# Kernel tuning notes

Hardware: AMD Instinct MI355X
Metric: run time of the kernel (lower is better)

Reference implementation:

```python
import jax, jax.numpy as jnp
import numpy as np

B, L, H, N, CIN, COUT, U = 32, 12, 12, 2048, 2, 1, 64
K3 = 3  # num_matrices = n_supports * max_diffusion_step + 1 = 1*2 + 1


def setup_inputs() -> dict:
    rng = np.random.default_rng(0)
    # random sparse-ish symmetric adjacency -> scaled laplacian support (lambda_max ~= 2)
    A = rng.random((N, N), dtype=np.float32)
    A = np.maximum(A, A.T)
    A = A * (A > 0.995)
    d = A.sum(axis=1)
    dis = 1.0 / np.sqrt(np.maximum(d, 1e-6))
    Lap = np.eye(N, dtype=np.float32) - (dis[:, None] * A) * dis[None, :]
    support = (Lap - np.eye(N, dtype=np.float32)).astype(np.float32)  # 2/lmax*L - I with lmax=2

    key = jax.random.key(0)
    ks = jax.random.split(key, 6)

    def w(k, shape, fan):
        return jax.random.normal(k, shape, jnp.float32) / np.float32(np.sqrt(fan))

    Cg_e = (CIN + U) * K3   # 198
    Cg_d = (COUT + U) * K3  # 195
    return {
        "history_data": jax.random.normal(ks[0], (B, L, N, CIN), jnp.float32),
        "support": jnp.asarray(support),
        "enc_Wg": w(ks[1], (Cg_e, 2 * U), Cg_e),
        "enc_bg": jnp.ones((2 * U,), jnp.float32),  # gate bias starts at 1.0 (original repo)
        "enc_Wc": w(ks[2], (Cg_e, U), Cg_e),
        "enc_bc": jnp.zeros((U,), jnp.float32),
        "dec_Wg": w(ks[3], (Cg_d, 2 * U), Cg_d),
        "dec_bg": jnp.ones((2 * U,), jnp.float32),
        "dec_Wc": w(ks[4], (Cg_d, U), Cg_d),
        "dec_bc": jnp.zeros((U,), jnp.float32),
        "Wp": w(ks[5], (U, COUT), U),
        "bp": jnp.zeros((COUT,), jnp.float32),
    }


def _gconv(support, x, W, b):
    # x: [B, N, C]; Chebyshev diffusion T0=x, T1=Sx, T2=2S(Sx)-x, stacked feature-major
    x1 = jnp.einsum('mn,bnc->bmc', support, x)
    x2 = 2.0 * jnp.einsum('mn,bnc->bmc', support, x1) - x
    xs = jnp.stack([x, x1, x2], axis=-1)  # [B, N, C, 3]
    b_, n_, c_, k_ = xs.shape
    y = xs.reshape(b_ * n_, c_ * k_) @ W + b
    return y.reshape(b_, n_, -1)


def _cell(support, x, h, Wg, bg, Wc, bc):
    # DCGRU cell: x [B,N,in], h [B,N,U]
    cat = jnp.concatenate([x, h], axis=-1)
    ru = jax.nn.sigmoid(_gconv(support, cat, Wg, bg))
    r, u = jnp.split(ru, 2, axis=-1)
    c = jnp.tanh(_gconv(support, jnp.concatenate([x, r * h], axis=-1), Wc, bc))
    return u * h + (1.0 - u) * c


def reference(history_data, support, enc_Wg, enc_bg, enc_Wc, enc_bc,
              dec_Wg, dec_bg, dec_Wc, dec_bc, Wp, bp):
    hist = jnp.transpose(history_data, (1, 0, 2, 3))  # [L, B, N, CIN]
    h0 = jnp.zeros((B, N, U), history_data.dtype)

    def enc_step(h, xt):
        return _cell(support, xt, h, enc_Wg, enc_bg, enc_Wc, enc_bc), None

    h_enc, _ = jax.lax.scan(enc_step, h0, hist)

    go = jnp.zeros((B, N, COUT), history_data.dtype)

    def dec_step(carry, _):
        h, xin = carry
        h = _cell(support, xin, h, dec_Wg, dec_bg, dec_Wc, dec_bc)
        out = (h.reshape(-1, U) @ Wp + bp).reshape(B, N, COUT)
        return (h, out), out

    _, outs = jax.lax.scan(dec_step, (h_enc, go), None, length=H)  # [H, B, N, COUT]
    return jnp.transpose(outs, (1, 0, 2, 3))  # [B, H, N, COUT]
```

## Files before the change

kernel.cpp:

```cpp
#include <hip/hip_runtime.h>
#include <math.h>

#define NN 2048
#define BB 32
#define LL 12
#define HHH 12
#define UU 64
#define STR 68
#define SLAB (BB*STR)
#define SEGP (SLAB/4)
#define MR (NN*BB)
#define CSR_CAP 262144
#define PACK_HALF 28672

typedef short bfrag __attribute__((ext_vector_type(8)));
typedef float ffrag __attribute__((ext_vector_type(4)));

__device__ __forceinline__ unsigned packsf(float x) {
  unsigned u = __float_as_uint(x);
  unsigned hb = (u + 0x7FFFu + ((u >> 16) & 1u)) & 0xFFFF0000u;
  float rem = x - __uint_as_float(hb);
  unsigned lb = __float_as_uint(rem) >> 16;
  return hb | lb;
}
__device__ __forceinline__ float recsf(unsigned u) {
  return __uint_as_float(u & 0xFFFF0000u) + __uint_as_float(u << 16);
}
__device__ __forceinline__ float sigm(float x) { return 1.0f / (1.0f + __expf(-x)); }
__device__ __forceinline__ float tanhfast(float x) {
  float e = __expf(2.0f * x);
  return 1.0f - 2.0f / (e + 1.0f);
}

__global__ __launch_bounds__(256) void k_row_count(const float* __restrict__ S, int* __restrict__ cnt) {
  int m = blockIdx.x;
  const float* row = S + (size_t)m * NN;
  int c = 0;
  for (int i = threadIdx.x; i < NN; i += 256) c += (row[i] != 0.0f);
  __shared__ int sm[4];
  for (int off = 32; off; off >>= 1) c += __shfl_down(c, off, 64);
  if ((threadIdx.x & 63) == 0) sm[threadIdx.x >> 6] = c;
  __syncthreads();
  if (threadIdx.x == 0) cnt[m] = sm[0] + sm[1] + sm[2] + sm[3];
}

__global__ __launch_bounds__(256) void k_scan(const int* __restrict__ cnt, int* __restrict__ rp) {
  __shared__ int tot[256];
  int t = threadIdx.x;
  int base = t * 8;
  int v[8]; int s = 0;
  #pragma unroll
  for (int k = 0; k < 8; ++k) { v[k] = cnt[base + k]; s += v[k]; }
  tot[t] = s;
  __syncthreads();
  for (int off = 1; off < 256; off <<= 1) {
    int add = (t >= off) ? tot[t - off] : 0;
    __syncthreads();
    tot[t] += add;
    __syncthreads();
  }
  int run = (t == 0) ? 0 : tot[t - 1];
  #pragma unroll
  for (int k = 0; k < 8; ++k) { rp[base + k] = run; run += v[k]; }
  if (t == 255) rp[NN] = run;
}

__global__ __launch_bounds__(256) void k_fill(const float* __restrict__ S, const int* __restrict__ rp,
                                              int* __restrict__ cols, float* __restrict__ vals) {
  int m = blockIdx.x;
  const float* row = S + (size_t)m * NN;
  __shared__ int wsum[4];
  __shared__ int chunkbase;
  if (threadIdx.x == 0) chunkbase = rp[m];
  __syncthreads();
  int lane = threadIdx.x & 63, w = threadIdx.x >> 6;
  for (int ch = 0; ch < NN / 256; ++ch) {
    int i = ch * 256 + threadIdx.x;
    float val = row[i];
    bool p = (val != 0.0f);
    unsigned long long mask = __ballot(p);
    int rank = __popcll(mask & ((1ull << lane) - 1ull));
    if (lane == 0) wsum[w] = __popcll(mask);
    __syncthreads();
    int off = 0;
    for (int q = 0; q < w; ++q) off += wsum[q];
    if (p) { int k = chunkbase + off + rank; cols[k] = i; vals[k] = val; }
    __syncthreads();
    if (threadIdx.x == 0) chunkbase += wsum[0] + wsum[1] + wsum[2] + wsum[3];
    __syncthreads();
  }
}

__global__ __launch_bounds__(256) void k_pack(const float* __restrict__ Wsrc, unsigned short* __restrict__ dst,
                                              int CIN_, int NO) {
  int idx = blockIdx.x * 256 + threadIdx.x;
  int nh_count = NO >> 6;
  int tot = nh_count * 7 * 4 * 64 * 8;
  if (idx >= tot) return;
  int j = idx & 7;
  int r1 = idx >> 3;  int lane = r1 & 63;
  int r2 = r1 >> 6;   int nf = r2 & 3;
  int r3 = r2 >> 2;   int ks = r3 % 7; int nh = r3 / 7;
  int grp = lane >> 4, l15 = lane & 15;
  int col = nh*64 + nf*16 + l15;
  float wv = 0.0f;
  if (ks < 6) {
    int kb = ks >> 1;
    int c = CIN_ + (ks & 1)*32 + grp*8 + j;
    wv = Wsrc[((size_t)c*3 + kb)*NO + col];
  } else {
    int q = grp*8 + j;
    if (q < 3*CIN_) { int kb = q / CIN_, c = q % CIN_; wv = Wsrc[((size_t)c*3 + kb)*NO + col]; }
  }
  unsigned pw = packsf(wv);
  size_t basehi = ((size_t)nh*PACK_HALF) + ((((size_t)ks*4 + nf)*2 + 0)*64 + lane)*8 + j;
  size_t baselo = ((size_t)nh*PACK_HALF) + ((((size_t)ks*4 + nf)*2 + 1)*64 + lane)*8 + j;
  dst[basehi] = (unsigned short)(pw >> 16);
  dst[baselo] = (unsigned short)(pw & 0xFFFFu);
}

__global__ __launch_bounds__(256) void k_packt(const float* __restrict__ src, unsigned* __restrict__ dst, int n) {
  int i = blockIdx.x * 256 + threadIdx.x;
  if (i < n) dst[i] = packsf(src[i]);
}

template<int SRC, int X0M>
__global__ __launch_bounds__(256, 4) void k_hop(
    const int* __restrict__ rp, const int* __restrict__ cols, const float* __restrict__ vals,
    const unsigned* __restrict__ src, const unsigned* __restrict__ xP,
    const unsigned* __restrict__ hP, const unsigned* __restrict__ x0p,
    unsigned* __restrict__ Y, int t) {
  __shared__ int   scol[64];
  __shared__ float sval[64];
  int orig = blockIdx.x;
  int swz = (orig & 7) * 1024 + (orig >> 3);
  int seg = swz >> 11;
  int node = swz & 2047;
  int j0 = rp[node], j1 = rp[node + 1];
  int tid = threadIdx.x;
  int w0 = seg * SEGP + tid, w1 = w0 + 256, w2 = w0 + 512;
  bool a2 = tid < (SEGP - 512);
  float acc0 = 0.f, acc1 = 0.f, acc2 = 0.f;

  int b0 = 0, c0 = 0, b1 = 0, c1 = 0, b2 = 0, c2 = 0;
  if constexpr (SRC != 0 || X0M > 0) {
    b0 = w0 / STR; c0 = w0 - b0 * STR;
    b1 = w1 / STR; c1 = w1 - b1 * STR;
    b2 = w2 / STR; c2 = w2 - b2 * STR;
  }

  const unsigned *bp0, *bp1, *bp2;
  unsigned st0, st1, st2;
  bool z0 = false, z1 = false, z2 = false;
  if constexpr (SRC == 0) {
    bp0 = src + w0; bp1 = src + w1; bp2 = src + (a2 ? w2 : w0);
    st0 = SLAB; st1 = SLAB; st2 = SLAB;
    z2 = !a2;
  } else {
    auto mk = [&](int b, int c, const unsigned*& bp, unsigned& st, bool& zz) {
      if (c < 64) { bp = hP + (size_t)b * UU + c; st = BB * UU; }
      else if (SRC == 1 && c < 66) { bp = xP + ((size_t)(b * LL + t)) * NN * 2 + (c - 64); st = 2; }
      else if (SRC == 2 && c == 64) { bp = xP + b; st = BB; }
      else { bp = hP; st = 0; zz = true; }
    };
    mk(b0, c0, bp0, st0, z0);
    mk(b1, c1, bp1, st1, z1);
    if (a2) mk(b2, c2, bp2, st2, z2);
    else { bp2 = hP; st2 = 0; z2 = true; }
  }

  for (int base = j0; base < j1; base += 64) {
    int cnt = min(64, j1 - base);
    if (tid < cnt) { scol[tid] = cols[base + tid]; sval[tid] = vals[base + tid]; }
    __syncthreads();
    int jj = 0;
    for (; jj + 4 <= cnt; jj += 4) {
      unsigned uv[12];
      float sv[4];
      #pragma unroll
      for (int q = 0; q < 4; ++q) {
        unsigned n = (unsigned)scol[jj + q];
        sv[q] = sval[jj + q];
        uv[q*3+0] = bp0[(size_t)(n * st0)];
        uv[q*3+1] = bp1[(size_t)(n * st1)];
        uv[q*3+2] = bp2[(size_t)(n * st2)];
      }
      #pragma unroll
      for (int q = 0; q < 4; ++q) {
        acc0 = fmaf(sv[q], recsf(z0 ? 0u : uv[q*3+0]), acc0);
        acc1 = fmaf(sv[q], recsf(z1 ? 0u : uv[q*3+1]), acc1);
        acc2 = fmaf(sv[q], recsf(z2 ? 0u : uv[q*3+2]), acc2);
      }
    }
    for (; jj < cnt; ++jj) {
      unsigned n = (unsigned)scol[jj]; float s = sval[jj];
      unsigned a = bp0[(size_t)(n * st0)];
      unsigned b = bp1[(size_t)(n * st1)];
      unsigned c = bp2[(size_t)(n * st2)];
      acc0 = fmaf(s, recsf(z0 ? 0u : a), acc0);
      acc1 = fmaf(s, recsf(z1 ? 0u : b), acc1);
      acc2 = fmaf(s, recsf(z2 ? 0u : c), acc2);
    }
    __syncthreads();
  }

  unsigned* yr = Y + (size_t)node * SLAB;
  if constexpr (X0M < 0) {
    yr[w0] = packsf(acc0);
    yr[w1] = packsf(acc1);
    if (a2) yr[w2] = packsf(acc2);
  } else {
    auto X0V = [&](int wq, int b, int c) -> float {
      if constexpr (X0M == 0) {
        return recsf(x0p[(size_t)node * SLAB + wq]);
      } else if constexpr (X0M == 1) {
        if (c < 64) return recsf(hP[((size_t)node * BB + b) * UU + c]);
        if (c < 66) return recsf(xP[(((size_t)(b * LL + t)) * NN + node) * 2 + (c - 64)]);
        return 0.f;
      } else {
        if (c < 64) return recsf(hP[((size_t)node * BB + b) * UU + c]);
        if (c == 64) return recsf(xP[(size_t)node * BB + b]);
        return 0.f;
      }
    };
    yr[w0] = packsf(2.f * acc0 - X0V(w0, b0, c0));
    yr[w1] = packsf(2.f * acc1 - X0V(w1, b1, c1));
    if (a2) yr[w2] = packsf(2.f * acc2 - X0V(w2, b2, c2));
  }
}

template<int CATM>
__global__ __launch_bounds__(256, 4) void k_gate(
    const unsigned* __restrict__ hP, const unsigned* __restrict__ xP,
    const unsigned* __restrict__ T1P, const unsigned* __restrict__ T2P,
    const unsigned short* __restrict__ Bpack, const float* __restrict__ bg,
    unsigned* __restrict__ zP, float* __restrict__ Ug, int t) {
  int tid = threadIdx.x;
  int r0 = blockIdx.x * 64;
  int w = tid >> 6, lane = tid & 63, grp = lane >> 4, l15 = lane & 15;
  int row0 = r0 + w*16 + l15;
  ffrag acc[8];
  #pragma unroll
  for (int nf = 0; nf < 8; ++nf) acc[nf] = (ffrag){0.f, 0.f, 0.f, 0.f};

  #pragma unroll
  for (int ks = 0; ks < 7; ++ks) {
    int ko = (ks & 1)*32 + grp*8;
    bfrag ah0, al0;
    if (ks < 6) {
      const unsigned* p0; int st;
      if (ks < 2)      { p0 = hP;  st = UU; }
      else if (ks < 4) { p0 = T1P; st = STR; }
      else             { p0 = T2P; st = STR; }
      const unsigned* a0 = p0 + (size_t)row0*st + ko;
      uint4 q00 = *(const uint4*)a0, q01 = *(const uint4*)(a0 + 4);
      unsigned ua0[8] = {q00.x,q00.y,q00.z,q00.w,q01.x,q01.y,q01.z,q01.w};
      #pragma unroll
      for (int jj = 0; jj < 8; ++jj) {
        ah0[jj] = (short)(ua0[jj] >> 16); al0[jj] = (short)(ua0[jj] & 0xFFFFu);
      }
    } else {
      unsigned ua0[8] = {0,0,0,0,0,0,0,0};
      if (grp == 0) {
        if (CATM == 1) {
          int n0r = row0 >> 5, b0r = row0 & 31;
          const unsigned* hx0 = xP + (((size_t)(b0r*LL + t))*NN + n0r)*2;
          ua0[0] = hx0[0]; ua0[1] = hx0[1];
          ua0[2] = T1P[(size_t)row0*STR + 64]; ua0[3] = T1P[(size_t)row0*STR + 65];
          ua0[4] = T2P[(size_t)row0*STR + 64]; ua0[5] = T2P[(size_t)row0*STR + 65];
        } else {
          ua0[0] = xP[row0];
          ua0[1] = T1P[(size_t)row0*STR + 64];
          ua0[2] = T2P[(size_t)row0*STR + 64];
        }
      }
      #pragma unroll
      for (int jj = 0; jj < 8; ++jj) {
        ah0[jj] = (short)(ua0[jj] >> 16); al0[jj] = (short)(ua0[jj] & 0xFFFFu);
      }
    }
    #pragma unroll
    for (int nf = 0; nf < 8; ++nf) {
      const unsigned short* bb = Bpack + (size_t)(nf >> 2)*PACK_HALF
                               + (((size_t)(ks*4 + (nf & 3))*2)*64 + lane)*8;
      bfrag bh = *(const bfrag*)bb;
      bfrag bl = *(const bfrag*)(bb + 512);
      acc[nf] = __builtin_amdgcn_mfma_f32_16x16x32_bf16(ah0, bh, acc[nf], 0, 0, 0);
      acc[nf] = __builtin_amdgcn_mfma_f32_16x16x32_bf16(ah0, bl, acc[nf], 0, 0, 0);
      acc[nf] = __builtin_amdgcn_mfma_f32_16x16x32_bf16(al0, bh, acc[nf], 0, 0, 0);
    }
  }
  float bgv[8];
  #pragma unroll
  for (int nf = 0; nf < 8; ++nf) bgv[nf] = bg[nf*16 + l15];
  #pragma unroll
  for (int reg = 0; reg < 4; ++reg) {
    int row = r0 + w*16 + grp*4 + reg;
    #pragma unroll
    for (int nf = 0; nf < 8; ++nf) {
      int col = nf*16 + l15;
      float v = sigm(acc[nf][reg] + bgv[nf]);
      if (col < 64) {
        float ho = recsf(hP[(size_t)row*UU + col]);
        zP[(size_t)row*STR + col] = packsf(v * ho);
      } else {
        Ug[(size_t)row*UU + (col - 64)] = v;
      }
    }
  }
  if (l15 == 0) {
    #pragma unroll
    for (int reg = 0; reg < 4; ++reg) {
      int row = r0 + w*16 + grp*4 + reg;
      size_t zb = (size_t)row*STR;
      if (CATM == 1) {
        int n = row >> 5, b = row & 31;
        const unsigned* hx = xP + (((size_t)(b*LL + t))*NN + n)*2;
        zP[zb + 64] = hx[0]; zP[zb + 65] = hx[1];
      } else {
        zP[zb + 64] = xP[row]; zP[zb + 65] = 0u;
      }
      zP[zb + 66] = 0u; zP[zb + 67] = 0u;
    }
  }
}

template<bool DEC>
__global__ __launch_bounds__(256, 4) void k_cand(
    const unsigned* __restrict__ zP, const unsigned* __restrict__ T1P,
    const unsigned* __restrict__ T2P,
    const unsigned short* __restrict__ Bpack, const float* __restrict__ bc,
    const float* __restrict__ Ug, const unsigned* __restrict__ hOld,
    unsigned* __restrict__ hNew,
    const float* __restrict__ Wp, const float* __restrict__ bp,
    float* __restrict__ out, unsigned* __restrict__ xioP, int t) {
  int tid = threadIdx.x;
  int r0 = blockIdx.x * 64;
  int w = tid >> 6, lane = tid & 63, grp = lane >> 4, l15 = lane & 15;
  int row0 = r0 + w*16 + l15;
  ffrag acc[4];
  #pragma unroll
  for (int nf = 0; nf < 4; ++nf) acc[nf] = (ffrag){0.f, 0.f, 0.f, 0.f};

  #pragma unroll
  for (int ks = 0; ks < 7; ++ks) {
    int ko = (ks & 1)*32 + grp*8;
    bfrag ah0, al0;
    if (ks < 6) {
      const unsigned* p0;
      if (ks < 2)      p0 = zP;
      else if (ks < 4) p0 = T1P;
      else             p0 = T2P;
      const unsigned* a0 = p0 + (size_t)row0*STR + ko;
      uint4 q00 = *(const uint4*)a0, q01 = *(const uint4*)(a0 + 4);
      unsigned ua0[8] = {q00.x,q00.y,q00.z,q00.w,q01.x,q01.y,q01.z,q01.w};
      #pragma unroll
      for (int jj = 0; jj < 8; ++jj) {
        ah0[jj] = (short)(ua0[jj] >> 16); al0[jj] = (short)(ua0[jj] & 0xFFFFu);
      }
    } else {
      unsigned ua0[8] = {0,0,0,0,0,0,0,0};
      if (grp == 0) {
        if (!DEC) {
          ua0[0] = zP[(size_t)row0*STR + 64];  ua0[1] = zP[(size_t)row0*STR + 65];
          ua0[2] = T1P[(size_t)row0*STR + 64]; ua0[3] = T1P[(size_t)row0*STR + 65];
          ua0[4] = T2P[(size_t)row0*STR + 64]; ua0[5] = T2P[(size_t)row0*STR + 65];
        } else {
          ua0[0] = zP[(size_t)row0*STR + 64];
          ua0[1] = T1P[(size_t)row0*STR + 64];
          ua0[2] = T2P[(size_t)row0*STR + 64];
        }
      }
      #pragma unroll
      for (int jj = 0; jj < 8; ++jj) {
        ah0[jj] = (short)(ua0[jj] >> 16); al0[jj] = (short)(ua0[jj] & 0xFFFFu);
      }
    }
    #pragma unroll
    for (int nf = 0; nf < 4; ++nf) {
      const unsigned short* bb = Bpack + (((size_t)(ks*4 + nf)*2)*64 + lane)*8;
      bfrag bh = *(const bfrag*)bb;
      bfrag bl = *(const bfrag*)(bb + 512);
      acc[nf] = __builtin_amdgcn_mfma_f32_16x16x32_bf16(ah0, bh, acc[nf], 0, 0, 0);
      acc[nf] = __builtin_amdgcn_mfma_f32_16x16x32_bf16(ah0, bl, acc[nf], 0, 0, 0);
      acc[nf] = __builtin_amdgcn_mfma_f32_16x16x32_bf16(al0, bh, acc[nf], 0, 0, 0);
    }
  }
  float bcv[4], wpv[4];
  #pragma unroll
  for (int nf = 0; nf < 4; ++nf) {
    bcv[nf] = bc[nf*16 + l15];
    wpv[nf] = DEC ? Wp[nf*16 + l15] : 0.f;
  }
  float bp0 = DEC ? bp[0] : 0.f;
  #pragma unroll
  for (int reg = 0; reg < 4; ++reg) {
    int row = r0 + w*16 + grp*4 + reg;
    float p = 0.f;
    #pragma unroll
    for (int nf = 0; nf < 4; ++nf) {
      int col = nf*16 + l15;
      float cf = tanhfast(acc[nf][reg] + bcv[nf]);
      float u  = Ug[(size_t)row*UU + col];
      float ho = recsf(hOld[(size_t)row*UU + col]);
      float hv = u * ho + (1.0f - u) * cf;
      hNew[(size_t)row*UU + col] = packsf(hv);
      if (DEC) p = fmaf(hv, wpv[nf], p);
    }
    if (DEC) {
      p += __shfl_xor(p, 1, 64);
      p += __shfl_xor(p, 2, 64);
      p += __shfl_xor(p, 4, 64);
      p += __shfl_xor(p, 8, 64);
      if (l15 == 0) {
        float val = p + bp0;
        int n = row >> 5, b = row & 31;
        out[((size_t)b*HHH + t)*NN + n] = val;
        xioP[row] = packsf(val);
      }
    }
  }
}

extern "C" void kernel_launch(void* const* d_in, const int* in_sizes, int n_in,
                              void* d_out, int out_size, void* d_ws, size_t ws_size,
                              hipStream_t stream) {
  (void)in_sizes; (void)n_in; (void)out_size; (void)ws_size;
  const float* hist = (const float*)d_in[0];
  const float* support = (const float*)d_in[1];
  const float* eWg = (const float*)d_in[2];
  const float* ebg = (const float*)d_in[3];
  const float* eWc = (const float*)d_in[4];
  const float* ebc = (const float*)d_in[5];
  const float* dWg = (const float*)d_in[6];
  const float* dbg = (const float*)d_in[7];
  const float* dWc = (const float*)d_in[8];
  const float* dbc = (const float*)d_in[9];
  const float* Wp  = (const float*)d_in[10];
  const float* bp  = (const float*)d_in[11];
  float* out = (float*)d_out;

  char* base = (char*)d_ws;
  size_t off = 0;
  auto carve = [&](size_t bytes) -> void* {
    void* p = base + off;
    off += (bytes + 255) & ~(size_t)255;
    return p;
  };
  int*   cnt   = (int*)carve(NN * 4);
  int*   rpB   = (int*)carve((NN + 1) * 4);
  int*   colsB = (int*)carve(CSR_CAP * 4);
  float* valsB = (float*)carve(CSR_CAP * 4);
  unsigned short* Pge = (unsigned short*)carve(2 * PACK_HALF * 2);
  unsigned short* Pgd = (unsigned short*)carve(2 * PACK_HALF * 2);
  unsigned short* Pce = (unsigned short*)carve((size_t)PACK_HALF * 2);
  unsigned short* Pcd = (unsigned short*)carve((size_t)PACK_HALF * 2);
  unsigned* histP = (unsigned*)carve((size_t)BB * LL * NN * 2 * 4);
  unsigned* T1P   = (unsigned*)carve((size_t)NN * SLAB * 4);
  unsigned* T2P   = (unsigned*)carve((size_t)NN * SLAB * 4);
  unsigned* zP    = (unsigned*)carve((size_t)NN * SLAB * 4);
  float*    UgF   = (float*)carve((size_t)MR * UU * 4);
  unsigned* hPa   = (unsigned*)carve((size_t)MR * UU * 4);
  unsigned* hPb   = (unsigned*)carve((size_t)MR * UU * 4);
  unsigned* xioP  = (unsigned*)carve((size_t)MR * 4);

  hipMemsetAsync(hPa, 0, (size_t)MR * UU * 4, stream);
  hipMemsetAsync(xioP, 0, (size_t)MR * 4, stream);

  k_row_count<<<NN, 256, 0, stream>>>(support, cnt);
  k_scan<<<1, 256, 0, stream>>>(cnt, rpB);
  k_fill<<<NN, 256, 0, stream>>>(support, rpB, colsB, valsB);
  k_pack<<<112, 256, 0, stream>>>(eWg, Pge, 2, 128);
  k_pack<<<56, 256, 0, stream>>>(eWc, Pce, 2, 64);
  k_pack<<<112, 256, 0, stream>>>(dWg, Pgd, 1, 128);
  k_pack<<<56, 256, 0, stream>>>(dWc, Pcd, 1, 64);
  k_packt<<<(BB*LL*NN*2 + 255)/256, 256, 0, stream>>>(hist, histP, BB*LL*NN*2);

  unsigned* hc = hPa; unsigned* hn = hPb;
  for (int t = 0; t < LL; ++t) {
    k_hop<1,-1><<<8192, 256, 0, stream>>>(rpB, colsB, valsB, nullptr, histP, hc, nullptr, T1P, t);
    k_hop<0, 1><<<8192, 256, 0, stream>>>(rpB, colsB, valsB, T1P, histP, hc, nullptr, T2P, t);
    k_gate<1><<<MR/64, 256, 0, stream>>>(hc, histP, T1P, T2P, Pge, ebg, zP, UgF, t);
    k_hop<0,-1><<<8192, 256, 0, stream>>>(rpB, colsB, valsB, zP, nullptr, nullptr, nullptr, T1P, t);
    k_hop<0, 0><<<8192, 256, 0, stream>>>(rpB, colsB, valsB, T1P, nullptr, nullptr, zP, T2P, t);
    k_cand<false><<<MR/64, 256, 0, stream>>>(zP, T1P, T2P, Pce, ebc, UgF, hc, hn,
                                             Wp, bp, out, xioP, t);
    unsigned* tmp = hc; hc = hn; hn = tmp;
  }
  for (int t = 0; t < HHH; ++t) {
    k_hop<2,-1><<<8192, 256, 0, stream>>>(rpB, colsB, valsB, nullptr, xioP, hc, nullptr, T1P, t);
    k_hop<0, 2><<<8192, 256, 0, stream>>>(rpB, colsB, valsB, T1P, xioP, hc, nullptr, T2P, t);
    k_gate<2><<<MR/64, 256, 0, stream>>>(hc, xioP, T1P, T2P, Pgd, dbg, zP, UgF, t);
    k_hop<0,-1><<<8192, 256, 0, stream>>>(rpB, colsB, valsB, zP, nullptr, nullptr, nullptr, T1P, t);
    k_hop<0, 0><<<8192, 256, 0, stream>>>(rpB, colsB, valsB, T1P, nullptr, nullptr, zP, T2P, t);
    k_cand<true><<<MR/64, 256, 0, stream>>>(zP, T1P, T2P, Pcd, dbc, UgF, hc, hn,
                                            Wp, bp, out, xioP, t);
    unsigned* tmp = hc; hc = hn; hn = tmp;
  }
}
```

Baseline: 3.971 ms.

## Fold Chebyshev 2Sx-x into packed weights and split hop into eight segments

The second diffusion hop now writes plain S·(Sx) rather than 2S(Sx)-x. The identity term and the factor of two are folded into the packed weight matrix: the T0 weight becomes W0-W2 and the T2 weight becomes 2·W2. This removes the per-element x0 reload and subtraction from the hop kernels. Separately, each node's slab is split into 8 segments instead of 4, giving 16384 blocks with two columns per thread and an 8-deep gather unroll. The goal is more parallelism and more memory-level parallelism, at the cost of more blocks re-reading the CSR row.

```diff
diff --git a/kernel.cpp b/kernel.cpp
--- a/kernel.cpp
+++ b/kernel.cpp
@@ -8,7 +8,8 @@
 #define UU 64
 #define STR 68
 #define SLAB (BB*STR)
-#define SEGP (SLAB/4)
+#define SEGS 8
+#define SEGW (SLAB/SEGS)
 #define MR (NN*BB)
 #define CSR_CAP 262144
 #define PACK_HALF 28672
@@ -104,13 +105,19 @@
   int grp = lane >> 4, l15 = lane & 15;
   int col = nh*64 + nf*16 + l15;
   float wv = 0.0f;
+  int kb = -1, c = 0;
   if (ks < 6) {
-    int kb = ks >> 1;
-    int c = CIN_ + (ks & 1)*32 + grp*8 + j;
-    wv = Wsrc[((size_t)c*3 + kb)*NO + col];
+    kb = ks >> 1;
+    c = CIN_ + (ks & 1)*32 + grp*8 + j;
   } else {
     int q = grp*8 + j;
-    if (q < 3*CIN_) { int kb = q / CIN_, c = q % CIN_; wv = Wsrc[((size_t)c*3 + kb)*NO + col]; }
+    if (q < 3*CIN_) { kb = q / CIN_; c = q % CIN_; }
+  }
+  if (kb >= 0) {
+    float w0 = Wsrc[((size_t)c*3 + 0)*NO + col];
+    float w1 = Wsrc[((size_t)c*3 + 1)*NO + col];
+    float w2 = Wsrc[((size_t)c*3 + 2)*NO + col];
+    wv = (kb == 0) ? (w0 - w2) : ((kb == 1) ? w1 : 2.0f*w2);
   }
   unsigned pw = packsf(wv);
   size_t basehi = ((size_t)nh*PACK_HALF) + ((((size_t)ks*4 + nf)*2 + 0)*64 + lane)*8 + j;
@@ -124,49 +131,41 @@
   if (i < n) dst[i] = packsf(src[i]);
 }
 
-template<int SRC, int X0M>
+template<int SRC>
 __global__ __launch_bounds__(256, 4) void k_hop(
     const int* __restrict__ rp, const int* __restrict__ cols, const float* __restrict__ vals,
     const unsigned* __restrict__ src, const unsigned* __restrict__ xP,
-    const unsigned* __restrict__ hP, const unsigned* __restrict__ x0p,
-    unsigned* __restrict__ Y, int t) {
+    const unsigned* __restrict__ hP, unsigned* __restrict__ Y, int t) {
   __shared__ int   scol[64];
   __shared__ float sval[64];
   int orig = blockIdx.x;
-  int swz = (orig & 7) * 1024 + (orig >> 3);
+  int swz = (orig & 7) * 2048 + (orig >> 3);
   int seg = swz >> 11;
   int node = swz & 2047;
   int j0 = rp[node], j1 = rp[node + 1];
   int tid = threadIdx.x;
-  int w0 = seg * SEGP + tid, w1 = w0 + 256, w2 = w0 + 512;
-  bool a2 = tid < (SEGP - 512);
-  float acc0 = 0.f, acc1 = 0.f, acc2 = 0.f;
-
-  int b0 = 0, c0 = 0, b1 = 0, c1 = 0, b2 = 0, c2 = 0;
-  if constexpr (SRC != 0 || X0M > 0) {
-    b0 = w0 / STR; c0 = w0 - b0 * STR;
-    b1 = w1 / STR; c1 = w1 - b1 * STR;
-    b2 = w2 / STR; c2 = w2 - b2 * STR;
-  }
-
-  const unsigned *bp0, *bp1, *bp2;
-  unsigned st0, st1, st2;
-  bool z0 = false, z1 = false, z2 = false;
+  int w0 = seg * SEGW + tid;
+  bool a1 = tid < (SEGW - 256);
+  int w1 = w0 + 256;
+  float acc0 = 0.f, acc1 = 0.f;
+
+  const unsigned *bp0, *bp1;
+  unsigned st0, st1;
+  bool z0 = false, z1 = false;
   if constexpr (SRC == 0) {
-    bp0 = src + w0; bp1 = src + w1; bp2 = src + (a2 ? w2 : w0);
-    st0 = SLAB; st1 = SLAB; st2 = SLAB;
-    z2 = !a2;
+    bp0 = src + w0; st0 = SLAB;
+    bp1 = src + (a1 ? w1 : w0); st1 = SLAB; z1 = !a1;
   } else {
-    auto mk = [&](int b, int c, const unsigned*& bp, unsigned& st, bool& zz) {
+    auto mk = [&](int wq, const unsigned*& bp, unsigned& st, bool& zz) {
+      int b = wq / STR, c = wq - b * STR;
       if (c < 64) { bp = hP + (size_t)b * UU + c; st = BB * UU; }
       else if (SRC == 1 && c < 66) { bp = xP + ((size_t)(b * LL + t)) * NN * 2 + (c - 64); st = 2; }
       else if (SRC == 2 && c == 64) { bp = xP + b; st = BB; }
       else { bp = hP; st = 0; zz = true; }
     };
-    mk(b0, c0, bp0, st0, z0);
-    mk(b1, c1, bp1, st1, z1);
-    if (a2) mk(b2, c2, bp2, st2, z2);
-    else { bp2 = hP; st2 = 0; z2 = true; }
+    mk(w0, bp0, st0, z0);
+    if (a1) mk(w1, bp1, st1, z1);
+    else { bp1 = hP; st1 = 0; z1 = true; }
   }
 
   for (int base = j0; base < j1; base += 64) {
@@ -174,59 +173,34 @@
     if (tid < cnt) { scol[tid] = cols[base + tid]; sval[tid] = vals[base + tid]; }
     __syncthreads();
     int jj = 0;
-    for (; jj + 4 <= cnt; jj += 4) {
-      unsigned uv[12];
-      float sv[4];
-      #pragma unroll
-      for (int q = 0; q < 4; ++q) {
+    for (; jj + 8 <= cnt; jj += 8) {
+      unsigned u0[8], u1[8];
+      float sv[8];
+      #pragma unroll
+      for (int q = 0; q < 8; ++q) {
         unsigned n = (unsigned)scol[jj + q];
         sv[q] = sval[jj + q];
-        uv[q*3+0] = bp0[(size_t)(n * st0)];
-        uv[q*3+1] = bp1[(size_t)(n * st1)];
-        uv[q*3+2] = bp2[(size_t)(n * st2)];
-      }
-      #pragma unroll
-      for (int q = 0; q < 4; ++q) {
-        acc0 = fmaf(sv[q], recsf(z0 ? 0u : uv[q*3+0]), acc0);
-        acc1 = fmaf(sv[q], recsf(z1 ? 0u : uv[q*3+1]), acc1);
-        acc2 = fmaf(sv[q], recsf(z2 ? 0u : uv[q*3+2]), acc2);
+        u0[q] = bp0[(size_t)(n * st0)];
+        u1[q] = bp1[(size_t)(n * st1)];
+      }
+      #pragma unroll
+      for (int q = 0; q < 8; ++q) {
+        acc0 = fmaf(sv[q], recsf(z0 ? 0u : u0[q]), acc0);
+        acc1 = fmaf(sv[q], recsf(z1 ? 0u : u1[q]), acc1);
       }
     }
     for (; jj < cnt; ++jj) {
       unsigned n = (unsigned)scol[jj]; float s = sval[jj];
       unsigned a = bp0[(size_t)(n * st0)];
       unsigned b = bp1[(size_t)(n * st1)];
-      unsigned c = bp2[(size_t)(n * st2)];
       acc0 = fmaf(s, recsf(z0 ? 0u : a), acc0);
       acc1 = fmaf(s, recsf(z1 ? 0u : b), acc1);
-      acc2 = fmaf(s, recsf(z2 ? 0u : c), acc2);
-    }
-    __syncthreads();
-  }
-
+    }
+    __syncthreads();
+  }
   unsigned* yr = Y + (size_t)node * SLAB;
-  if constexpr (X0M < 0) {
-    yr[w0] = packsf(acc0);
-    yr[w1] = packsf(acc1);
-    if (a2) yr[w2] = packsf(acc2);
-  } else {
-    auto X0V = [&](int wq, int b, int c) -> float {
-      if constexpr (X0M == 0) {
-        return recsf(x0p[(size_t)node * SLAB + wq]);
-      } else if constexpr (X0M == 1) {
-        if (c < 64) return recsf(hP[((size_t)node * BB + b) * UU + c]);
-        if (c < 66) return recsf(xP[(((size_t)(b * LL + t)) * NN + node) * 2 + (c - 64)]);
-        return 0.f;
-      } else {
-        if (c < 64) return recsf(hP[((size_t)node * BB + b) * UU + c]);
-        if (c == 64) return recsf(xP[(size_t)node * BB + b]);
-        return 0.f;
-      }
-    };
-    yr[w0] = packsf(2.f * acc0 - X0V(w0, b0, c0));
-    yr[w1] = packsf(2.f * acc1 - X0V(w1, b1, c1));
-    if (a2) yr[w2] = packsf(2.f * acc2 - X0V(w2, b2, c2));
-  }
+  yr[w0] = packsf(acc0);
+  if (a1) yr[w1] = packsf(acc1);
 }
 
 template<int CATM>
@@ -478,21 +452,21 @@
 
   unsigned* hc = hPa; unsigned* hn = hPb;
   for (int t = 0; t < LL; ++t) {
-    k_hop<1,-1><<<8192, 256, 0, stream>>>(rpB, colsB, valsB, nullptr, histP, hc, nullptr, T1P, t);
-    k_hop<0, 1><<<8192, 256, 0, stream>>>(rpB, colsB, valsB, T1P, histP, hc, nullptr, T2P, t);
+    k_hop<1><<<NN*SEGS, 256, 0, stream>>>(rpB, colsB, valsB, nullptr, histP, hc, T1P, t);
+    k_hop<0><<<NN*SEGS, 256, 0, stream>>>(rpB, colsB, valsB, T1P, nullptr, nullptr, T2P, t);
     k_gate<1><<<MR/64, 256, 0, stream>>>(hc, histP, T1P, T2P, Pge, ebg, zP, UgF, t);
-    k_hop<0,-1><<<8192, 256, 0, stream>>>(rpB, colsB, valsB, zP, nullptr, nullptr, nullptr, T1P, t);
-    k_hop<0, 0><<<8192, 256, 0, stream>>>(rpB, colsB, valsB, T1P, nullptr, nullptr, zP, T2P, t);
+    k_hop<0><<<NN*SEGS, 256, 0, stream>>>(rpB, colsB, valsB, zP, nullptr, nullptr, T1P, t);
+    k_hop<0><<<NN*SEGS, 256, 0, stream>>>(rpB, colsB, valsB, T1P, nullptr, nullptr, T2P, t);
     k_cand<false><<<MR/64, 256, 0, stream>>>(zP, T1P, T2P, Pce, ebc, UgF, hc, hn,
                                              Wp, bp, out, xioP, t);
     unsigned* tmp = hc; hc = hn; hn = tmp;
   }
   for (int t = 0; t < HHH; ++t) {
-    k_hop<2,-1><<<8192, 256, 0, stream>>>(rpB, colsB, valsB, nullptr, xioP, hc, nullptr, T1P, t);
-    k_hop<0, 2><<<8192, 256, 0, stream>>>(rpB, colsB, valsB, T1P, xioP, hc, nullptr, T2P, t);
+    k_hop<2><<<NN*SEGS, 256, 0, stream>>>(rpB, colsB, valsB, nullptr, xioP, hc, T1P, t);
+    k_hop<0><<<NN*SEGS, 256, 0, stream>>>(rpB, colsB, valsB, T1P, nullptr, nullptr, T2P, t);
     k_gate<2><<<MR/64, 256, 0, stream>>>(hc, xioP, T1P, T2P, Pgd, dbg, zP, UgF, t);
-    k_hop<0,-1><<<8192, 256, 0, stream>>>(rpB, colsB, valsB, zP, nullptr, nullptr, nullptr, T1P, t);
-    k_hop<0, 0><<<8192, 256, 0, stream>>>(rpB, colsB, valsB, T1P, nullptr, nullptr, zP, T2P, t);
+    k_hop<0><<<NN*SEGS, 256, 0, stream>>>(rpB, colsB, valsB, zP, nullptr, nullptr, T1P, t);
+    k_hop<0><<<NN*SEGS, 256, 0, stream>>>(rpB, colsB, valsB, T1P, nullptr, nullptr, T2P, t);
     k_cand<true><<<MR/64, 256, 0, stream>>>(zP, T1P, T2P, Pcd, dbc, UgF, hc, hn,
                                             Wp, bp, out, xioP, t);
     unsigned* tmp = hc; hc = hn; hn = tmp;
```

New measurement: 4.588 ms. 15.5% more time.
